# Kernel tuning notes

Measured on AMD Instinct MI355X. Metric: run time of the kernel, lower is better.

## Reference

```python
import jax, jax.numpy as jnp
import numpy as np
from jax import lax

K = 20
EPS = 1e-5
SLOPE = 0.2


def knn_idx(x, k):
    # x: [B, C, N] -> idx [B, N, k] of nearest neighbors (incl. self)
    inner = jnp.einsum('bcn,bcm->bnm', x, x)
    sq = jnp.sum(x * x, axis=1)                      # [B, N]
    neg_d = -(sq[:, :, None] + sq[:, None, :] - 2.0 * inner)
    _, idx = lax.top_k(neg_d, k)
    return idx


def graph_feature(x, idx):
    # x: [B, C, N], idx: [B, N, k] -> [B, 2C, N, k]
    B = x.shape[0]
    xt = jnp.transpose(x, (0, 2, 1))                 # [B, N, C]
    neigh = xt[jnp.arange(B)[:, None, None], idx]    # [B, N, k, C]
    center = jnp.broadcast_to(xt[:, :, None, :], neigh.shape)
    feat = jnp.concatenate([neigh - center, center], axis=-1)  # [B, N, k, 2C]
    return jnp.transpose(feat, (0, 3, 1, 2))         # [B, 2C, N, k]


def conv_bn_lrelu(feat, W, gamma, beta):
    # 1x1 Conv2d (no bias) + eval-mode BN (mean=0, var=1) + LeakyReLU(0.2)
    y = jnp.einsum('oc,bcnk->bonk', W, feat)
    scale = gamma / jnp.sqrt(1.0 + EPS)
    y = y * scale[None, :, None, None] + beta[None, :, None, None]
    return jnp.where(y >= 0, y, SLOPE * y)


def setup_inputs() -> dict:
    key = jax.random.key(0)
    ks = jax.random.split(key, 16)
    B, N, emb = 4, 2048, 1024
    d = {'x': jax.random.normal(ks[0], (B, 3, N), dtype=jnp.float32)}
    dims = [(64, 6), (64, 128), (128, 128), (256, 256), (emb, 256)]
    for i, (o, c) in enumerate(dims):
        d[f'W{i+1}'] = jax.random.normal(ks[1 + i], (o, c), dtype=jnp.float32) * (1.0 / np.sqrt(c))
        d[f'g{i+1}'] = 1.0 + 0.1 * jax.random.normal(ks[6 + i], (o,), dtype=jnp.float32)
        d[f'b{i+1}'] = 0.1 * jax.random.normal(ks[11 + i], (o,), dtype=jnp.float32)
    return d


def reference(x, W1, W2, W3, W4, W5, g1, g2, g3, g4, g5, b1, b2, b3, b4, b5):
    # EdgeConv block 1
    f = graph_feature(x, knn_idx(x, K))              # [B, 6, N, k]
    x1 = jnp.max(conv_bn_lrelu(f, W1, g1, b1), axis=-1)   # [B, 64, N]
    # EdgeConv block 2
    f = graph_feature(x1, knn_idx(x1, K))            # [B, 128, N, k]
    x2 = jnp.max(conv_bn_lrelu(f, W2, g2, b2), axis=-1)   # [B, 64, N]
    # EdgeConv block 3
    f = graph_feature(x2, knn_idx(x2, K))            # [B, 128, N, k]
    x3 = jnp.max(conv_bn_lrelu(f, W3, g3, b3), axis=-1)   # [B, 128, N]
    # EdgeConv block 4
    f = graph_feature(x3, knn_idx(x3, K))            # [B, 256, N, k]
    x4 = jnp.max(conv_bn_lrelu(f, W4, g4, b4), axis=-1)   # [B, 256, N]
    # conv5 (1x1 over points) + global max pool
    x5 = conv_bn_lrelu(x4[:, :, :, None], W5, g5, b5)     # [B, emb, N, 1]
    return jnp.max(x5[..., 0], axis=-1)              # [B, emb]
```

## Files before the change

### kernel.cpp

```cpp
#include <hip/hip_runtime.h>
#include <math.h>

#define BB 4
#define NN 2048
#define KK 20

static __device__ __forceinline__ float lrelu(float z) {
    return z >= 0.f ? z : 0.2f * z;
}

template<int CTRL>
static __device__ __forceinline__ unsigned dpp_min_step(unsigned v) {
    unsigned t = (unsigned)__builtin_amdgcn_update_dpp(
        (int)0xFFFFFFFFu, (int)v, CTRL, 0xF, 0xF, false);
    return v < t ? v : t;
}
static __device__ __forceinline__ unsigned wave_min_bcast(unsigned v) {
    v = dpp_min_step<0x111>(v);
    v = dpp_min_step<0x112>(v);
    v = dpp_min_step<0x114>(v);
    v = dpp_min_step<0x118>(v);
    v = dpp_min_step<0x142>(v);
    v = dpp_min_step<0x143>(v);
    return (unsigned)__builtin_amdgcn_readlane((int)v, 63);
}

template<int C>
__global__ __launch_bounds__(256) void sq_kernel(const float* __restrict__ x,
                                                 float* __restrict__ sq) {
    int i = blockIdx.x * 256 + threadIdx.x;
    if (i >= BB * NN) return;
    int b = i / NN, n = i - b * NN;
    const float* xb = x + (size_t)b * C * NN + n;
    float s = 0.f;
    #pragma unroll
    for (int c = 0; c < C; ++c) {
        float v = xb[(size_t)c * NN];
        s = fmaf(v, v, s);
    }
    sq[i] = s;
}

template<int C>
__global__ __launch_bounds__(256, 4) void knn_kernel(const float* __restrict__ x,
                                                     const float* __restrict__ sq,
                                                     int* __restrict__ idx) {
    const int QT = 4;
    __shared__ unsigned dl[QT][NN];
    __shared__ float xq[QT][C];
    __shared__ float sqq[QT];
    int blk = blockIdx.x;
    int b = blk / (NN / QT);
    int q0 = (blk - b * (NN / QT)) * QT;
    int t = threadIdx.x;
    int lane = t & 63, wid = t >> 6;

    const float* xb = x + (size_t)b * C * NN;
    for (int e = t; e < QT * C; e += 256) {
        int q = e / C, c = e - q * C;
        xq[q][c] = xb[(size_t)c * NN + q0 + q];
    }
    if (t < QT) sqq[t] = sq[b * NN + q0 + t];
    __syncthreads();

    float acc[QT][8];
    #pragma unroll
    for (int q = 0; q < QT; ++q)
        #pragma unroll
        for (int s = 0; s < 8; ++s) acc[q][s] = 0.f;

    for (int c = 0; c < C; ++c) {
        float xj[8];
        #pragma unroll
        for (int s = 0; s < 8; ++s) xj[s] = xb[(size_t)c * NN + t + s * 256];
        #pragma unroll
        for (int q = 0; q < QT; ++q) {
            float xqc = xq[q][c];
            #pragma unroll
            for (int s = 0; s < 8; ++s) acc[q][s] = fmaf(xqc, xj[s], acc[q][s]);
        }
    }
    float sqj[8];
    #pragma unroll
    for (int s = 0; s < 8; ++s) sqj[s] = sq[b * NN + t + s * 256];

    #pragma unroll
    for (int q = 0; q < QT; ++q) {
        float sqi = sqq[q];
        #pragma unroll
        for (int s = 0; s < 8; ++s) {
            float d = sqi + sqj[s] - 2.f * acc[q][s];
            unsigned u = __float_as_uint(d);
            unsigned key = u ^ ((unsigned)((int)u >> 31) | 0x80000000u);
            int j = s * 256 + t;
            int w = (j & ~31) | ((((j >> 2) ^ (j >> 5)) & 7) << 2) | (j & 3);
            dl[q][w] = key;
        }
    }
    __syncthreads();

    unsigned* dq = &dl[wid][0];
    int r7 = lane & 7;
    int lanebase = lane << 5;
    const uint4* cp0 = (const uint4*)(dq + lanebase + ((0 ^ r7) << 2));
    const uint4* cp1 = (const uint4*)(dq + lanebase + ((1 ^ r7) << 2));
    const uint4* cp2 = (const uint4*)(dq + lanebase + ((2 ^ r7) << 2));
    const uint4* cp3 = (const uint4*)(dq + lanebase + ((3 ^ r7) << 2));
    const uint4* cp4 = (const uint4*)(dq + lanebase + ((4 ^ r7) << 2));
    const uint4* cp5 = (const uint4*)(dq + lanebase + ((5 ^ r7) << 2));
    const uint4* cp6 = (const uint4*)(dq + lanebase + ((6 ^ r7) << 2));
    const uint4* cp7 = (const uint4*)(dq + lanebase + ((7 ^ r7) << 2));

    int* orow = idx + (size_t)(b * NN + q0 + wid) * KK;
    #pragma unroll 1
    for (int rr = 0; rr < KK; ++rr) {
        uint4 v0 = *cp0, v1 = *cp1, v2 = *cp2, v3 = *cp3;
        uint4 v4 = *cp4, v5 = *cp5, v6 = *cp6, v7 = *cp7;
        unsigned ck[8]; int cs[8];
#define CHUNK(i, V) {                                                   \
        unsigned kA = (V.y < V.x) ? V.y : V.x;                          \
        int      sA = 4*(i) + ((V.y < V.x) ? 1 : 0);                    \
        unsigned kB = (V.w < V.z) ? V.w : V.z;                          \
        int      sB = 4*(i) + 2 + ((V.w < V.z) ? 1 : 0);                \
        bool w2 = kB < kA;                                              \
        ck[i] = w2 ? kB : kA; cs[i] = w2 ? sB : sA; }
        CHUNK(0, v0) CHUNK(1, v1) CHUNK(2, v2) CHUNK(3, v3)
        CHUNK(4, v4) CHUNK(5, v5) CHUNK(6, v6) CHUNK(7, v7)
#undef CHUNK
        unsigned k01 = ck[1] < ck[0] ? ck[1] : ck[0];
        int      s01 = ck[1] < ck[0] ? cs[1] : cs[0];
        unsigned k23 = ck[3] < ck[2] ? ck[3] : ck[2];
        int      s23 = ck[3] < ck[2] ? cs[3] : cs[2];
        unsigned k45 = ck[5] < ck[4] ? ck[5] : ck[4];
        int      s45 = ck[5] < ck[4] ? cs[5] : cs[4];
        unsigned k67 = ck[7] < ck[6] ? ck[7] : ck[6];
        int      s67 = ck[7] < ck[6] ? cs[7] : cs[6];
        unsigned k03 = k23 < k01 ? k23 : k01;
        int      s03 = k23 < k01 ? s23 : s01;
        unsigned k47 = k67 < k45 ? k67 : k45;
        int      s47 = k67 < k45 ? s67 : s45;
        bool wf = k47 < k03;
        unsigned kf = wf ? k47 : k03;
        int      sf = wf ? s47 : s03;

        unsigned g = wave_min_bcast(kf);
        unsigned encl = (kf == g) ? (unsigned)(lanebase + sf) : 0xFFFFFFFFu;
        unsigned j = wave_min_bcast(encl);
        if (lane == 0) orow[rr] = (int)j;
        if ((int)(j >> 5) == lane) {
            int lo = (int)j & 31;
            dq[lanebase + (((lo >> 2) ^ r7) << 2) + (lo & 3)] = 0xFFFFFFFFu;
        }
    }
}

template<int C, int OT>
__global__ __launch_bounds__(256) void pt_kernel(const float* __restrict__ x,
                                                 const float* __restrict__ W,
                                                 float* __restrict__ p,
                                                 float* __restrict__ tt,
                                                 int O) {
    const int NB = NN / 256;
    int blk = blockIdx.x;
    int nb = blk % NB;
    int rest = blk / NB;
    int nob = O / OT;
    int ob = rest % nob;
    int b = rest / nob;
    int t = threadIdx.x;
    int n = nb * 256 + t;
    __shared__ float wn[OT][C], wd[OT][C];
    for (int e = t; e < OT * C; e += 256) {
        int o = e / C, c = e - o * C;
        float a = W[(size_t)(ob * OT + o) * (2 * C) + c];
        float b2 = W[(size_t)(ob * OT + o) * (2 * C) + C + c];
        wn[o][c] = a;
        wd[o][c] = b2 - a;
    }
    __syncthreads();
    float ap[OT], at[OT];
    #pragma unroll
    for (int o = 0; o < OT; ++o) { ap[o] = 0.f; at[o] = 0.f; }
    const float* xb = x + (size_t)b * C * NN + n;
    for (int c = 0; c < C; ++c) {
        float xv = xb[(size_t)c * NN];
        #pragma unroll
        for (int o = 0; o < OT; ++o) {
            ap[o] = fmaf(wn[o][c], xv, ap[o]);
            at[o] = fmaf(wd[o][c], xv, at[o]);
        }
    }
    size_t base = ((size_t)b * O + ob * OT) * NN + n;
    #pragma unroll
    for (int o = 0; o < OT; ++o) {
        p[base + (size_t)o * NN] = ap[o];
        tt[base + (size_t)o * NN] = at[o];
    }
}

__global__ __launch_bounds__(256) void edge_kernel(const float* __restrict__ p,
                                                   const float* __restrict__ tt,
                                                   const int* __restrict__ idx,
                                                   const float* __restrict__ g,
                                                   const float* __restrict__ be,
                                                   float* __restrict__ out, int O) {
    int b = blockIdx.x / O, o = blockIdx.x - b * O;
    __shared__ float pl[NN];
    const float* pr = p + ((size_t)b * O + o) * NN;
    for (int e = threadIdx.x * 4; e < NN; e += 1024)
        *(float4*)&pl[e] = *(const float4*)&pr[e];
    __syncthreads();
    float scale = g[o] / sqrtf(1.f + 1e-5f);
    float beta = be[o];
    const float* tr = tt + ((size_t)b * O + o) * NN;
    float* orow = out + ((size_t)b * O + o) * NN;
    for (int i = threadIdx.x; i < NN; i += 256) {
        float ti = tr[i];
        const int4* ir4 = (const int4*)(idx + (size_t)(b * NN + i) * KK);
        int4 w0 = ir4[0], w1 = ir4[1], w2 = ir4[2], w3 = ir4[3], w4 = ir4[4];
        float m = -__builtin_inff();
        int js[20] = {w0.x, w0.y, w0.z, w0.w, w1.x, w1.y, w1.z, w1.w,
                      w2.x, w2.y, w2.z, w2.w, w3.x, w3.y, w3.z, w3.w,
                      w4.x, w4.y, w4.z, w4.w};
        #pragma unroll
        for (int k = 0; k < KK; ++k) {
            float y = pl[js[k]] + ti;
            m = fmaxf(m, lrelu(fmaf(scale, y, beta)));
        }
        orow[i] = m;
    }
}

__global__ __launch_bounds__(256) void transpose_kernel(const float* __restrict__ W,
                                                        float* __restrict__ WT) {
    __shared__ float tile[32][33];
    int c0 = blockIdx.x * 32, o0 = blockIdx.y * 32;
    int tx = threadIdx.x, ty = threadIdx.y;
    #pragma unroll
    for (int i = 0; i < 32; i += 8)
        tile[ty + i][tx] = W[(size_t)(o0 + ty + i) * 256 + c0 + tx];
    __syncthreads();
    #pragma unroll
    for (int i = 0; i < 32; i += 8)
        WT[(size_t)(c0 + ty + i) * 1024 + o0 + tx] = tile[tx][ty + i];
}

__global__ __launch_bounds__(256) void final_kernel(const float* __restrict__ x4,
                                                    const float* __restrict__ W5T,
                                                    const float* __restrict__ g,
                                                    const float* __restrict__ be,
                                                    float* __restrict__ partial) {
    const int CC = 256;
    __shared__ float xs[64][64];
    __shared__ float ws[64][64];
    int blk = blockIdx.x;
    int nb = blk & 31;
    int ob = (blk >> 5) & 15;
    int b  = blk >> 9;
    int t = threadIdx.x;
    int tn = t & 15, to = t >> 4;

    float acc[4][4];
    #pragma unroll
    for (int i = 0; i < 4; ++i)
        #pragma unroll
        for (int j = 0; j < 4; ++j) acc[i][j] = 0.f;

    for (int c0 = 0; c0 < CC; c0 += 64) {
        __syncthreads();
        #pragma unroll
        for (int e = t * 4; e < 64 * 64; e += 1024) {
            int c = e >> 6, n = e & 63;
            *(float4*)&xs[c][n] =
                *(const float4*)&x4[((size_t)b * CC + c0 + c) * NN + nb * 64 + n];
        }
        #pragma unroll
        for (int e = t * 4; e < 64 * 64; e += 1024) {
            int c = e >> 6, o = e & 63;
            *(float4*)&ws[c][o] =
                *(const float4*)&W5T[(size_t)(c0 + c) * 1024 + ob * 64 + o];
        }
        __syncthreads();
        for (int c = 0; c < 64; ++c) {
            float4 xv = *(float4*)&xs[c][tn * 4];
            float4 wv = *(float4*)&ws[c][to * 4];
            acc[0][0] = fmaf(wv.x, xv.x, acc[0][0]);
            acc[0][1] = fmaf(wv.x, xv.y, acc[0][1]);
            acc[0][2] = fmaf(wv.x, xv.z, acc[0][2]);
            acc[0][3] = fmaf(wv.x, xv.w, acc[0][3]);
            acc[1][0] = fmaf(wv.y, xv.x, acc[1][0]);
            acc[1][1] = fmaf(wv.y, xv.y, acc[1][1]);
            acc[1][2] = fmaf(wv.y, xv.z, acc[1][2]);
            acc[1][3] = fmaf(wv.y, xv.w, acc[1][3]);
            acc[2][0] = fmaf(wv.z, xv.x, acc[2][0]);
            acc[2][1] = fmaf(wv.z, xv.y, acc[2][1]);
            acc[2][2] = fmaf(wv.z, xv.z, acc[2][2]);
            acc[2][3] = fmaf(wv.z, xv.w, acc[2][3]);
            acc[3][0] = fmaf(wv.w, xv.x, acc[3][0]);
            acc[3][1] = fmaf(wv.w, xv.y, acc[3][1]);
            acc[3][2] = fmaf(wv.w, xv.z, acc[3][2]);
            acc[3][3] = fmaf(wv.w, xv.w, acc[3][3]);
        }
    }

    float rs = 1.f / sqrtf(1.f + 1e-5f);
    #pragma unroll
    for (int i = 0; i < 4; ++i) {
        int o = ob * 64 + to * 4 + i;
        float scale = g[o] * rs, beta = be[o];
        float m = -__builtin_inff();
        #pragma unroll
        for (int j = 0; j < 4; ++j)
            m = fmaxf(m, lrelu(fmaf(scale, acc[i][j], beta)));
        #pragma unroll
        for (int off = 8; off >= 1; off >>= 1)
            m = fmaxf(m, __shfl_xor(m, off));
        if (tn == 0)
            partial[(size_t)(nb * BB + b) * 1024 + o] = m;
    }
}

__global__ __launch_bounds__(256) void reduce32_kernel(const float* __restrict__ partial,
                                                       float* __restrict__ out) {
    int i = blockIdx.x * 256 + threadIdx.x;
    if (i >= BB * 1024) return;
    int b = i >> 10, o = i & 1023;
    float m = -__builtin_inff();
    #pragma unroll
    for (int nb = 0; nb < 32; ++nb)
        m = fmaxf(m, partial[(size_t)(nb * BB + b) * 1024 + o]);
    out[i] = m;
}

extern "C" void kernel_launch(void* const* d_in, const int* in_sizes, int n_in,
                              void* d_out, int out_size, void* d_ws, size_t ws_size,
                              hipStream_t stream) {
    const float* x  = (const float*)d_in[0];
    const float* W1 = (const float*)d_in[1];
    const float* g1 = (const float*)d_in[2];
    const float* b1 = (const float*)d_in[3];
    const float* W2 = (const float*)d_in[4];
    const float* g2 = (const float*)d_in[5];
    const float* b2 = (const float*)d_in[6];
    const float* W3 = (const float*)d_in[7];
    const float* g3 = (const float*)d_in[8];
    const float* b3 = (const float*)d_in[9];
    const float* W4 = (const float*)d_in[10];
    const float* g4 = (const float*)d_in[11];
    const float* b4 = (const float*)d_in[12];
    const float* W5 = (const float*)d_in[13];
    const float* g5 = (const float*)d_in[14];
    const float* b5 = (const float*)d_in[15];

    float* ws = (float*)d_ws;
    float* sq      = ws;
    int*   idx     = (int*)(ws + 8192);
    float* x1      = ws + 8192 + 163840;
    float* x2      = x1 + 524288;
    float* x3      = x2 + 524288;
    float* x4      = x3 + 1048576;
    float* p       = x4 + 2097152;
    float* tt      = p + 2097152;
    float* W5T     = p;
    float* partial = tt;

    dim3 blk(256);

    sq_kernel<3><<<32, blk, 0, stream>>>(x, sq);
    knn_kernel<3><<<BB * (NN / 4), blk, 0, stream>>>(x, sq, idx);
    pt_kernel<3, 16><<<BB * (64 / 16) * (NN / 256), blk, 0, stream>>>(x, W1, p, tt, 64);
    edge_kernel<<<BB * 64, blk, 0, stream>>>(p, tt, idx, g1, b1, x1, 64);

    sq_kernel<64><<<32, blk, 0, stream>>>(x1, sq);
    knn_kernel<64><<<BB * (NN / 4), blk, 0, stream>>>(x1, sq, idx);
    pt_kernel<64, 16><<<BB * (64 / 16) * (NN / 256), blk, 0, stream>>>(x1, W2, p, tt, 64);
    edge_kernel<<<BB * 64, blk, 0, stream>>>(p, tt, idx, g2, b2, x2, 64);

    sq_kernel<64><<<32, blk, 0, stream>>>(x2, sq);
    knn_kernel<64><<<BB * (NN / 4), blk, 0, stream>>>(x2, sq, idx);
    pt_kernel<64, 16><<<BB * (128 / 16) * (NN / 256), blk, 0, stream>>>(x2, W3, p, tt, 128);
    edge_kernel<<<BB * 128, blk, 0, stream>>>(p, tt, idx, g3, b3, x3, 128);

    sq_kernel<128><<<32, blk, 0, stream>>>(x3, sq);
    knn_kernel<128><<<BB * (NN / 4), blk, 0, stream>>>(x3, sq, idx);
    pt_kernel<128, 16><<<BB * (256 / 16) * (NN / 256), blk, 0, stream>>>(x3, W4, p, tt, 256);
    edge_kernel<<<BB * 256, blk, 0, stream>>>(p, tt, idx, g4, b4, x4, 256);

    transpose_kernel<<<dim3(8, 32), dim3(32, 8), 0, stream>>>(W5, W5T);
    final_kernel<<<BB * 16 * 32, blk, 0, stream>>>(x4, W5T, g5, b5, partial);
    reduce32_kernel<<<16, blk, 0, stream>>>(partial, (float*)d_out);
}
```

Baseline: 636.7 us.

## Replace per-round LDS rescan with per-lane top-4 register heap in kNN select

The kNN top-k selection used to rescan all 32 LDS keys per lane and run two wave-wide min reductions for each of the 20 rounds. Each lane now keeps a sorted top-4 list of packed (key, index) 64-bit values in registers. It does one 64-bit wave min per round and rescans its LDS slice only when its local list runs dry, using the last popped value as a threshold. This cuts LDS traffic and halves the reduction count, but the 64-bit DPP reduction costs more per step and the per-element insertion logic branches.

```diff
diff --git a/kernel.cpp b/kernel.cpp
--- a/kernel.cpp
+++ b/kernel.cpp
@@ -4,25 +4,31 @@
 #define BB 4
 #define NN 2048
 #define KK 20
+#define INFPK 0xFFFFFFFFFFFFFFFFull
 
 static __device__ __forceinline__ float lrelu(float z) {
     return z >= 0.f ? z : 0.2f * z;
 }
 
 template<int CTRL>
-static __device__ __forceinline__ unsigned dpp_min_step(unsigned v) {
-    unsigned t = (unsigned)__builtin_amdgcn_update_dpp(
-        (int)0xFFFFFFFFu, (int)v, CTRL, 0xF, 0xF, false);
-    return v < t ? v : t;
-}
-static __device__ __forceinline__ unsigned wave_min_bcast(unsigned v) {
-    v = dpp_min_step<0x111>(v);
-    v = dpp_min_step<0x112>(v);
-    v = dpp_min_step<0x114>(v);
-    v = dpp_min_step<0x118>(v);
-    v = dpp_min_step<0x142>(v);
-    v = dpp_min_step<0x143>(v);
-    return (unsigned)__builtin_amdgcn_readlane((int)v, 63);
+static __device__ __forceinline__ unsigned long long dpp_min64_step(unsigned long long v) {
+    unsigned lo = (unsigned)__builtin_amdgcn_update_dpp(
+        (int)0xFFFFFFFFu, (int)(unsigned)v, CTRL, 0xF, 0xF, false);
+    unsigned hi = (unsigned)__builtin_amdgcn_update_dpp(
+        (int)0xFFFFFFFFu, (int)(unsigned)(v >> 32), CTRL, 0xF, 0xF, false);
+    unsigned long long t = ((unsigned long long)hi << 32) | lo;
+    return t < v ? t : v;
+}
+static __device__ __forceinline__ unsigned long long wave_min64_bcast(unsigned long long v) {
+    v = dpp_min64_step<0x111>(v);
+    v = dpp_min64_step<0x112>(v);
+    v = dpp_min64_step<0x114>(v);
+    v = dpp_min64_step<0x118>(v);
+    v = dpp_min64_step<0x142>(v);
+    v = dpp_min64_step<0x143>(v);
+    unsigned lo = (unsigned)__builtin_amdgcn_readlane((int)(unsigned)v, 63);
+    unsigned hi = (unsigned)__builtin_amdgcn_readlane((int)(unsigned)(v >> 32), 63);
+    return ((unsigned long long)hi << 32) | lo;
 }
 
 template<int C>
@@ -102,56 +108,70 @@
     unsigned* dq = &dl[wid][0];
     int r7 = lane & 7;
     int lanebase = lane << 5;
-    const uint4* cp0 = (const uint4*)(dq + lanebase + ((0 ^ r7) << 2));
-    const uint4* cp1 = (const uint4*)(dq + lanebase + ((1 ^ r7) << 2));
-    const uint4* cp2 = (const uint4*)(dq + lanebase + ((2 ^ r7) << 2));
-    const uint4* cp3 = (const uint4*)(dq + lanebase + ((3 ^ r7) << 2));
-    const uint4* cp4 = (const uint4*)(dq + lanebase + ((4 ^ r7) << 2));
-    const uint4* cp5 = (const uint4*)(dq + lanebase + ((5 ^ r7) << 2));
-    const uint4* cp6 = (const uint4*)(dq + lanebase + ((6 ^ r7) << 2));
-    const uint4* cp7 = (const uint4*)(dq + lanebase + ((7 ^ r7) << 2));
+
+    unsigned long long h0 = INFPK, h1 = INFPK, h2 = INFPK, h3 = INFPK;
+
+#define PK_INS(KEY, LO) {                                                     \
+        unsigned long long v =                                                \
+            ((unsigned long long)(KEY) << 12) | (unsigned)(lanebase + (LO));  \
+        if (v < h3) {                                                         \
+            unsigned long long nh3 = h2 > v ? h2 : v;                         \
+            unsigned long long t2  = h2 < v ? h2 : v;                         \
+            unsigned long long nh2 = h1 > t2 ? h1 : t2;                       \
+            unsigned long long t1  = h1 < v ? h1 : v;                         \
+            unsigned long long nh1 = h0 > t1 ? h0 : t1;                       \
+            unsigned long long nh0 = h0 < v ? h0 : v;                         \
+            h0 = nh0; h1 = nh1; h2 = nh2; h3 = nh3;                           \
+        } }
+#define PK_INS_THR(KEY, LO) {                                                 \
+        unsigned long long v =                                                \
+            ((unsigned long long)(KEY) << 12) | (unsigned)(lanebase + (LO));  \
+        if (v > thr && v < h3) {                                              \
+            unsigned long long nh3 = h2 > v ? h2 : v;                         \
+            unsigned long long t2  = h2 < v ? h2 : v;                         \
+            unsigned long long nh2 = h1 > t2 ? h1 : t2;                       \
+            unsigned long long t1  = h1 < v ? h1 : v;                         \
+            unsigned long long nh1 = h0 > t1 ? h0 : t1;                       \
+            unsigned long long nh0 = h0 < v ? h0 : v;                         \
+            h0 = nh0; h1 = nh1; h2 = nh2; h3 = nh3;                           \
+        } }
+#define CHUNK_RD(c) uint4 V##c = *(const uint4*)(dq + lanebase + (((c) ^ r7) << 2));
+#define CHUNK_INS(c)     { PK_INS(V##c.x, 4*(c)+0) PK_INS(V##c.y, 4*(c)+1)        \
+                           PK_INS(V##c.z, 4*(c)+2) PK_INS(V##c.w, 4*(c)+3) }
+#define CHUNK_INS_THR(c) { PK_INS_THR(V##c.x, 4*(c)+0) PK_INS_THR(V##c.y, 4*(c)+1) \
+                           PK_INS_THR(V##c.z, 4*(c)+2) PK_INS_THR(V##c.w, 4*(c)+3) }
+
+    {
+        CHUNK_RD(0) CHUNK_RD(1) CHUNK_RD(2) CHUNK_RD(3)
+        CHUNK_RD(4) CHUNK_RD(5) CHUNK_RD(6) CHUNK_RD(7)
+        CHUNK_INS(0) CHUNK_INS(1) CHUNK_INS(2) CHUNK_INS(3)
+        CHUNK_INS(4) CHUNK_INS(5) CHUNK_INS(6) CHUNK_INS(7)
+    }
 
     int* orow = idx + (size_t)(b * NN + q0 + wid) * KK;
+    unsigned long long thr = 0;
+    int popped = 0;
     #pragma unroll 1
     for (int rr = 0; rr < KK; ++rr) {
-        uint4 v0 = *cp0, v1 = *cp1, v2 = *cp2, v3 = *cp3;
-        uint4 v4 = *cp4, v5 = *cp5, v6 = *cp6, v7 = *cp7;
-        unsigned ck[8]; int cs[8];
-#define CHUNK(i, V) {                                                   \
-        unsigned kA = (V.y < V.x) ? V.y : V.x;                          \
-        int      sA = 4*(i) + ((V.y < V.x) ? 1 : 0);                    \
-        unsigned kB = (V.w < V.z) ? V.w : V.z;                          \
-        int      sB = 4*(i) + 2 + ((V.w < V.z) ? 1 : 0);                \
-        bool w2 = kB < kA;                                              \
-        ck[i] = w2 ? kB : kA; cs[i] = w2 ? sB : sA; }
-        CHUNK(0, v0) CHUNK(1, v1) CHUNK(2, v2) CHUNK(3, v3)
-        CHUNK(4, v4) CHUNK(5, v5) CHUNK(6, v6) CHUNK(7, v7)
-#undef CHUNK
-        unsigned k01 = ck[1] < ck[0] ? ck[1] : ck[0];
-        int      s01 = ck[1] < ck[0] ? cs[1] : cs[0];
-        unsigned k23 = ck[3] < ck[2] ? ck[3] : ck[2];
-        int      s23 = ck[3] < ck[2] ? cs[3] : cs[2];
-        unsigned k45 = ck[5] < ck[4] ? ck[5] : ck[4];
-        int      s45 = ck[5] < ck[4] ? cs[5] : cs[4];
-        unsigned k67 = ck[7] < ck[6] ? ck[7] : ck[6];
-        int      s67 = ck[7] < ck[6] ? cs[7] : cs[6];
-        unsigned k03 = k23 < k01 ? k23 : k01;
-        int      s03 = k23 < k01 ? s23 : s01;
-        unsigned k47 = k67 < k45 ? k67 : k45;
-        int      s47 = k67 < k45 ? s67 : s45;
-        bool wf = k47 < k03;
-        unsigned kf = wf ? k47 : k03;
-        int      sf = wf ? s47 : s03;
-
-        unsigned g = wave_min_bcast(kf);
-        unsigned encl = (kf == g) ? (unsigned)(lanebase + sf) : 0xFFFFFFFFu;
-        unsigned j = wave_min_bcast(encl);
-        if (lane == 0) orow[rr] = (int)j;
-        if ((int)(j >> 5) == lane) {
-            int lo = (int)j & 31;
-            dq[lanebase + (((lo >> 2) ^ r7) << 2) + (lo & 3)] = 0xFFFFFFFFu;
-        }
-    }
+        unsigned long long g = wave_min64_bcast(h0);
+        if (lane == 0) orow[rr] = (int)(g & 0xFFFu);
+        if (h0 == g) {
+            thr = g;
+            ++popped;
+            h0 = h1; h1 = h2; h2 = h3; h3 = INFPK;
+            if (h0 == INFPK && popped < 32) {
+                CHUNK_RD(0) CHUNK_RD(1) CHUNK_RD(2) CHUNK_RD(3)
+                CHUNK_RD(4) CHUNK_RD(5) CHUNK_RD(6) CHUNK_RD(7)
+                CHUNK_INS_THR(0) CHUNK_INS_THR(1) CHUNK_INS_THR(2) CHUNK_INS_THR(3)
+                CHUNK_INS_THR(4) CHUNK_INS_THR(5) CHUNK_INS_THR(6) CHUNK_INS_THR(7)
+            }
+        }
+    }
+#undef PK_INS
+#undef PK_INS_THR
+#undef CHUNK_RD
+#undef CHUNK_INS
+#undef CHUNK_INS_THR
 }
 
 template<int C, int OT>
```

After: 588.8 us. -7.5%, faster.
